# Optimization experiments

Hardware: AMD Instinct MI355X
Metric: run time of the kernel (lower is better)

The kernel has to match this reference:

```python
import jax, jax.numpy as jnp
import numpy as np

N = 200_000   # nodes
E = 6_400_000 # edges (avg degree 32)
G = 1024      # graphs in the batch
H = 8         # hidden dim


def setup_inputs() -> dict:
    key = jax.random.key(0)
    ks = jax.random.split(key, 13)
    x = jax.random.normal(ks[0], (N, 1), dtype=jnp.float32)
    edge_index = jax.random.randint(ks[1], (2, E), 0, N, dtype=jnp.int32)
    batch = jnp.sort(jax.random.randint(ks[2], (N,), 0, G, dtype=jnp.int32))
    s = 0.3
    params = dict(
        W1a=s * jax.random.normal(ks[3], (1, H), jnp.float32),
        b1a=jnp.zeros((H,), jnp.float32),
        W1b=s * jax.random.normal(ks[4], (H, H), jnp.float32),
        b1b=jnp.zeros((H,), jnp.float32),
        W2a=s * jax.random.normal(ks[5], (H, H), jnp.float32),
        b2a=jnp.zeros((H,), jnp.float32),
        W2b=s * jax.random.normal(ks[6], (H, H), jnp.float32),
        b2b=jnp.zeros((H,), jnp.float32),
        Wfc=s * jax.random.normal(ks[7], (H, 1), jnp.float32),
        bfc=jnp.zeros((1,), jnp.float32),
    )
    return dict(x=x, edge_index=edge_index, batch=batch, **params)


def _gin_layer(h, src, dst, Wa, ba, Wb, bb):
    # GINConv with eps=0: mlp(x_i + sum_{j->i} x_j); messages aggregated at dst=edge_index[1]
    agg = jax.ops.segment_sum(h[src], dst, num_segments=N)  # [N, d]
    z = h + agg
    z = jax.nn.relu(z @ Wa + ba)
    return z @ Wb + bb


def reference(x, edge_index, batch, W1a, b1a, W1b, b1b, W2a, b2a, W2b, b2b, Wfc, bfc):
    src, dst = edge_index[0], edge_index[1]
    h = _gin_layer(x, src, dst, W1a, b1a, W1b, b1b)   # [N, 8]
    h = jax.nn.elu(h)
    h = _gin_layer(h, src, dst, W2a, b2a, W2b, b2b)   # [N, 8]
    # global mean pool over graphs
    sums = jax.ops.segment_sum(h, batch, num_segments=G)                  # [G, 8]
    counts = jax.ops.segment_sum(jnp.ones((N,), h.dtype), batch, num_segments=G)
    pooled = sums / jnp.maximum(counts, 1.0)[:, None]
    out = jax.nn.sigmoid(pooled @ Wfc + bfc)          # [G, 1]
    return out.reshape(-1)
```

## Files before the change

kernel.cpp:

```cpp
#include <hip/hip_runtime.h>
#include <hip/hip_fp8.h>
#include <math.h>

#define H 8
#define NBLKA 256
#define BTH 1024
#define BSH 8
#define BCAP 9216
#define TS 1024
#define CAP 14336
#define SCAP 25600
#define POOLG 128

__device__ __forceinline__ unsigned f2fp8(float f) {
    __hip_fp8_e4m3 q(f);
    return (unsigned)q.__x;
}
__device__ __forceinline__ float fp8f(unsigned v) {
    __hip_fp8_e4m3 q;
    q.__x = (__hip_fp8_storage_t)v;
    return (float)q;
}
#if defined(__has_builtin)
#if __has_builtin(__builtin_amdgcn_cvt_pk_f32_fp8)
#define HAVE_CVT_PK_FP8 1
#endif
#endif
typedef float v2f __attribute__((ext_vector_type(2)));
__device__ __forceinline__ void unpack8(float* f, uint2 v) {
#ifdef HAVE_CVT_PK_FP8
    v2f f01 = __builtin_amdgcn_cvt_pk_f32_fp8((int)v.x, false);
    v2f f23 = __builtin_amdgcn_cvt_pk_f32_fp8((int)v.x, true);
    v2f f45 = __builtin_amdgcn_cvt_pk_f32_fp8((int)v.y, false);
    v2f f67 = __builtin_amdgcn_cvt_pk_f32_fp8((int)v.y, true);
    f[0] = f01.x; f[1] = f01.y; f[2] = f23.x; f[3] = f23.y;
    f[4] = f45.x; f[5] = f45.y; f[6] = f67.x; f[7] = f67.y;
#else
    f[0] = fp8f(v.x & 255u);         f[1] = fp8f((v.x >> 8) & 255u);
    f[2] = fp8f((v.x >> 16) & 255u); f[3] = fp8f(v.x >> 24);
    f[4] = fp8f(v.y & 255u);         f[5] = fp8f((v.y >> 8) & 255u);
    f[6] = fp8f((v.y >> 16) & 255u); f[7] = fp8f(v.y >> 24);
#endif
}
__device__ __forceinline__ void acc8(float* a, uint2 v) {
    float f[8];
    unpack8(f, v);
#pragma unroll
    for (int j = 0; j < 8; j++) a[j] += f[j];
}

__global__ __launch_bounds__(BTH) void scatterK(const int* __restrict__ ei, int E, int NB,
                                                int chunk, int* __restrict__ cursor,
                                                unsigned* __restrict__ packed) {
    __shared__ unsigned ss[SCAP];
    __shared__ int cnt[1024], sc[1024], base[1024], cur[1024];
    int t = threadIdx.x, blk = blockIdx.x;
    cnt[t] = 0;
    __syncthreads();
    int s = blk * chunk, e = min(E, s + chunk);
    for (int i = s + t; i < e; i += BTH)
        atomicAdd(&cnt[__builtin_nontemporal_load(ei + E + i) >> BSH], 1);
    __syncthreads();
    int c = cnt[t];
    sc[t] = c;
    __syncthreads();
    for (int off = 1; off < 1024; off <<= 1) {
        int v = (t >= off) ? sc[t - off] : 0;
        __syncthreads();
        sc[t] += v;
        __syncthreads();
    }
    cur[t] = sc[t] - c;
    base[t] = (t < NB && c > 0) ? atomicAdd(&cursor[t], c) : 0;
    __syncthreads();
    for (int i = s + t; i < e; i += BTH) {
        int src = __builtin_nontemporal_load(ei + i);
        int dst = __builtin_nontemporal_load(ei + E + i);
        int pos = atomicAdd(&cur[dst >> BSH], 1);
        ss[pos] = ((unsigned)src << 8) | (unsigned)(dst & 255);
    }
    __syncthreads();
    int wave = t >> 6, lane = t & 63;
    for (int j = wave; j < NB; j += (BTH >> 6)) {
        int n = cnt[j];
        int ls = sc[j] - n;
        int bs = base[j];
        int m = min(n, BCAP - bs);
        int gs = j * BCAP + bs;
        for (int k = lane; k < m; k += 64)
            packed[gs + k] = ss[ls + k];
    }
}

__global__ __launch_bounds__(TS, 8) void sortL1K(
                        unsigned* __restrict__ packed, const int* __restrict__ bucketCnt,
                        const float* __restrict__ x, int N,
                        const float* __restrict__ W1a, const float* __restrict__ b1a,
                        const float* __restrict__ W1b, const float* __restrict__ b1b,
                        int* __restrict__ nodeStart, uint2* __restrict__ h1) {
    __shared__ unsigned ss[CAP];
    __shared__ int cnt[256], sb[256], cur[256];
    __shared__ float sW1a[H], sb1a[H], sW1b[H * H], sb1b[H];
    int t = threadIdx.x, b = blockIdx.x;
    if (t < 256) cnt[t] = 0;
    else if (t < 256 + H) { int j = t - 256; sW1a[j] = W1a[j]; sb1a[j] = b1a[j]; sb1b[j] = b1b[j]; }
    else if (t < 256 + H + H * H) { int j = t - 256 - H; sW1b[j] = W1b[j]; }
    __syncthreads();
    int s = b * BCAP;
    int n_e = min(bucketCnt[b], BCAP);
    for (int i = t; i < n_e; i += TS)
        atomicAdd(&cnt[__builtin_nontemporal_load(packed + s + i) & 255u], 1);
    __syncthreads();
    if (t < 256) sb[t] = cnt[t];
    __syncthreads();
    for (int off = 1; off < 256; off <<= 1) {
        int add = (t < 256 && t >= off) ? sb[t - off] : 0;
        __syncthreads();
        if (t < 256) sb[t] += add;
        __syncthreads();
    }
    if (t < 256) {
        int excl = sb[t] - cnt[t];
        cur[t] = excl;
        nodeStart[(b << BSH) + t] = s + excl;
    }
    __syncthreads();
    for (int i = t; i < n_e; i += TS) {
        unsigned p = __builtin_nontemporal_load(packed + s + i);
        int pos = atomicAdd(&cur[p & 255u], 1);
        ss[pos] = p >> 8;
    }
    __syncthreads();
    for (int i = t; i < n_e; i += TS) packed[s + i] = ss[i];
    int node = t >> 2, q4 = t & 3;
    int gn = (b << BSH) + node;
    float xself = x[min(gn, N - 1)];
    int lo = sb[node] - cnt[node], hi = sb[node];
    float sum = 0.f;
    for (int k0 = lo + q4; k0 < hi; k0 += 32) {
        unsigned i0 = ss[k0];
        unsigned i1 = ss[min(k0 + 4,  hi - 1)];
        unsigned i2 = ss[min(k0 + 8,  hi - 1)];
        unsigned i3 = ss[min(k0 + 12, hi - 1)];
        unsigned i4 = ss[min(k0 + 16, hi - 1)];
        unsigned i5 = ss[min(k0 + 20, hi - 1)];
        unsigned i6 = ss[min(k0 + 24, hi - 1)];
        unsigned i7 = ss[min(k0 + 28, hi - 1)];
        float x0 = x[i0], x1 = x[i1], x2 = x[i2], x3 = x[i3];
        float x4 = x[i4], x5 = x[i5], x6 = x[i6], x7 = x[i7];
        sum += x0;
        if (k0 + 4  < hi) sum += x1;
        if (k0 + 8  < hi) sum += x2;
        if (k0 + 12 < hi) sum += x3;
        if (k0 + 16 < hi) sum += x4;
        if (k0 + 20 < hi) sum += x5;
        if (k0 + 24 < hi) sum += x6;
        if (k0 + 28 < hi) sum += x7;
    }
    sum += __shfl_xor(sum, 1, 64);
    sum += __shfl_xor(sum, 2, 64);
    if (q4 == 0 && gn < N) {
        float z = xself + sum;
        float tv[H];
#pragma unroll
        for (int k = 0; k < H; k++) tv[k] = fmaxf(fmaf(z, sW1a[k], sb1a[k]), 0.f);
        float hv[H];
#pragma unroll
        for (int j = 0; j < H; j++) {
            float a = sb1b[j];
#pragma unroll
            for (int k = 0; k < H; k++) a += tv[k] * sW1b[k * H + j];
            hv[j] = a > 0.f ? a : (expf(a) - 1.f);
        }
        uint2 o;
        o.x = f2fp8(hv[0]) | (f2fp8(hv[1]) << 8) | (f2fp8(hv[2]) << 16) | (f2fp8(hv[3]) << 24);
        o.y = f2fp8(hv[4]) | (f2fp8(hv[5]) << 8) | (f2fp8(hv[6]) << 16) | (f2fp8(hv[7]) << 24);
        h1[gn] = o;
    }
}

__global__ __launch_bounds__(1024, 8) void layer2K(
        const unsigned* __restrict__ packed, const int* __restrict__ nodeStart,
        const int* __restrict__ bucketCnt, const uint2* __restrict__ h1, int N,
        const float* __restrict__ W2a, const float* __restrict__ b2a,
        const float* __restrict__ W2b, const float* __restrict__ b2b,
        const int* __restrict__ batch, float* __restrict__ sumsCnt) {
    __shared__ unsigned ss[BCAP];
    __shared__ int sNS[257];
    __shared__ float pool[POOLG * 9];
    __shared__ float sW2a[H * H], sb2a[H], sW2b[H * H], sb2b[H];
    int t = threadIdx.x, b = blockIdx.x;
    int s = b * BCAP;
    int n_e = min(bucketCnt[b], BCAP);
    for (int i = t; i < n_e; i += 1024)
        ss[i] = __builtin_nontemporal_load(packed + s + i);
    if (t < 256) sNS[t] = nodeStart[(b << BSH) + t] - s;
    if (t == 256) sNS[256] = 0;
    if (t < H) { sb2a[t] = b2a[t]; sb2b[t] = b2b[t]; }
    else if (t >= 64 && t < 64 + H * H) sW2a[t - 64] = W2a[t - 64];
    else if (t >= 192 && t < 192 + H * H) sW2b[t - 192] = W2b[t - 192];
    __syncthreads();
    if (t == 0) sNS[256] = n_e;
    __syncthreads();
    int node = t >> 2, q4 = t & 3;
    int gn = (b << BSH) + node;
    uint2 vself = h1[gn];
    int lo = sNS[node], hi = sNS[node + 1];
    float a[H] = {0.f, 0.f, 0.f, 0.f, 0.f, 0.f, 0.f, 0.f};
    for (int k0 = lo + q4; k0 < hi; k0 += 32) {
        unsigned i0 = ss[k0];
        unsigned i1 = ss[min(k0 + 4,  hi - 1)];
        unsigned i2 = ss[min(k0 + 8,  hi - 1)];
        unsigned i3 = ss[min(k0 + 12, hi - 1)];
        unsigned i4 = ss[min(k0 + 16, hi - 1)];
        unsigned i5 = ss[min(k0 + 20, hi - 1)];
        unsigned i6 = ss[min(k0 + 24, hi - 1)];
        unsigned i7 = ss[min(k0 + 28, hi - 1)];
        uint2 v0 = h1[i0];
        uint2 v1 = h1[i1];
        uint2 v2 = h1[i2];
        uint2 v3 = h1[i3];
        uint2 v4 = h1[i4];
        uint2 v5 = h1[i5];
        uint2 v6 = h1[i6];
        uint2 v7 = h1[i7];
        acc8(a, v0);
        if (k0 + 4  < hi) acc8(a, v1);
        if (k0 + 8  < hi) acc8(a, v2);
        if (k0 + 12 < hi) acc8(a, v3);
        if (k0 + 16 < hi) acc8(a, v4);
        if (k0 + 20 < hi) acc8(a, v5);
        if (k0 + 24 < hi) acc8(a, v6);
        if (k0 + 28 < hi) acc8(a, v7);
    }
#pragma unroll
    for (int j = 0; j < H; j++) {
        a[j] += __shfl_xor(a[j], 1, 64);
        a[j] += __shfl_xor(a[j], 2, 64);
    }
    bool valid = (q4 == 0) && (gn < N);
    float h2[H];
    int g = 0;
    if (valid) {
        float zs[H];
        unpack8(zs, vself);
        float z[H];
#pragma unroll
        for (int j = 0; j < H; j++) z[j] = zs[j] + a[j];
        float tv[H];
#pragma unroll
        for (int k = 0; k < H; k++) {
            float acc = sb2a[k];
#pragma unroll
            for (int j = 0; j < H; j++) acc += z[j] * sW2a[j * H + k];
            tv[k] = fmaxf(acc, 0.f);
        }
#pragma unroll
        for (int j = 0; j < H; j++) {
            float acc = sb2b[j];
#pragma unroll
            for (int k = 0; k < H; k++) acc += tv[k] * sW2b[k * H + j];
            h2[j] = acc;
        }
        g = batch[gn];
    }
    int gfirst = batch[min(b << BSH, N - 1)];
    int glast  = batch[min((b << BSH) + 255, N - 1)];
    int span = glast - gfirst + 1;
    if (span <= POOLG) {
        int span9 = span * 9;
        for (int j = t; j < span9; j += 1024) pool[j] = 0.f;
        __syncthreads();
        if (valid) {
            float* p = &pool[(g - gfirst) * 9];
#pragma unroll
            for (int j = 0; j < H; j++) atomicAdd(p + j, h2[j]);
            atomicAdd(p + 8, 1.f);
        }
        __syncthreads();
        for (int j = t; j < span9; j += 1024)
            atomicAdd(&sumsCnt[(size_t)gfirst * 9 + j], pool[j]);
    } else if (valid) {
        float* p = &sumsCnt[(size_t)g * 9];
#pragma unroll
        for (int j = 0; j < H; j++) atomicAdd(p + j, h2[j]);
        atomicAdd(p + 8, 1.f);
    }
}

__global__ void finalK(const float* __restrict__ sumsCnt, const float* __restrict__ Wfc,
                       const float* __restrict__ bfc, float* __restrict__ out, int G) {
    int g = blockIdx.x * blockDim.x + threadIdx.x;
    if (g >= G) return;
    const float* s = &sumsCnt[(size_t)g * 9];
    float c = fmaxf(s[8], 1.f);
    float dot = 0.f;
#pragma unroll
    for (int j = 0; j < H; j++) dot += s[j] * Wfc[j];
    float a = dot / c + bfc[0];
    out[g] = 1.f / (1.f + expf(-a));
}

__global__ void edge_agg1(const int* __restrict__ ei, const float* __restrict__ x,
                          float* __restrict__ agg1, int E) {
    int e = blockIdx.x * blockDim.x + threadIdx.x;
    if (e >= E) return;
    atomicAdd(&agg1[ei[E + e]], x[ei[e]]);
}
__global__ void node1F(const float* __restrict__ x, const float* __restrict__ agg1,
                       const float* __restrict__ W1a, const float* __restrict__ b1a,
                       const float* __restrict__ W1b, const float* __restrict__ b1b,
                       float* __restrict__ h1, int N) {
    int n = blockIdx.x * blockDim.x + threadIdx.x;
    if (n >= N) return;
    float z = x[n] + agg1[n];
    float tv[H];
#pragma unroll
    for (int k = 0; k < H; k++) tv[k] = fmaxf(z * W1a[k] + b1a[k], 0.f);
#pragma unroll
    for (int j = 0; j < H; j++) {
        float acc = b1b[j];
#pragma unroll
        for (int k = 0; k < H; k++) acc += tv[k] * W1b[k * H + j];
        h1[(size_t)n * H + j] = acc > 0.f ? acc : (expf(acc) - 1.f);
    }
}
__global__ void edge_agg2(const int* __restrict__ ei, const float* __restrict__ h1,
                          float* __restrict__ agg2, int E) {
    long long i = (long long)blockIdx.x * blockDim.x + threadIdx.x;
    if (i >= (long long)E * H) return;
    int e = (int)(i >> 3), k = (int)(i & 7);
    atomicAdd(&agg2[(size_t)ei[E + e] * H + k], h1[(size_t)ei[e] * H + k]);
}
__global__ void node2F(const float* __restrict__ h1, const float* __restrict__ agg2,
                       const float* __restrict__ W2a, const float* __restrict__ b2a,
                       const float* __restrict__ W2b, const float* __restrict__ b2b,
                       const int* __restrict__ batch,
                       float* __restrict__ sums, float* __restrict__ counts, int N) {
    int n = blockIdx.x * blockDim.x + threadIdx.x;
    if (n >= N) return;
    float z[H], tv[H];
#pragma unroll
    for (int j = 0; j < H; j++) z[j] = h1[(size_t)n * H + j] + agg2[(size_t)n * H + j];
#pragma unroll
    for (int k = 0; k < H; k++) {
        float a = b2a[k];
#pragma unroll
        for (int j = 0; j < H; j++) a += z[j] * W2a[j * H + k];
        tv[k] = fmaxf(a, 0.f);
    }
    int g = batch[n];
#pragma unroll
    for (int j = 0; j < H; j++) {
        float a = b2b[j];
#pragma unroll
        for (int k = 0; k < H; k++) a += tv[k] * W2b[k * H + j];
        atomicAdd(&sums[(size_t)g * H + j], a);
    }
    atomicAdd(&counts[g], 1.f);
}
__global__ void finalF(const float* __restrict__ sums, const float* __restrict__ counts,
                       const float* __restrict__ Wfc, const float* __restrict__ bfc,
                       float* __restrict__ out, int G) {
    int g = blockIdx.x * blockDim.x + threadIdx.x;
    if (g >= G) return;
    float c = fmaxf(counts[g], 1.f);
    float acc = bfc[0];
#pragma unroll
    for (int j = 0; j < H; j++) acc += (sums[(size_t)g * H + j] / c) * Wfc[j];
    out[g] = 1.f / (1.f + expf(-acc));
}

extern "C" void kernel_launch(void* const* d_in, const int* in_sizes, int n_in,
                              void* d_out, int out_size, void* d_ws, size_t ws_size,
                              hipStream_t stream) {
    const float* x    = (const float*)d_in[0];
    const int*   ei   = (const int*)d_in[1];
    const int*   batch= (const int*)d_in[2];
    const float* W1a  = (const float*)d_in[3];
    const float* b1a  = (const float*)d_in[4];
    const float* W1b  = (const float*)d_in[5];
    const float* b1b  = (const float*)d_in[6];
    const float* W2a  = (const float*)d_in[7];
    const float* b2a  = (const float*)d_in[8];
    const float* W2b  = (const float*)d_in[9];
    const float* b2b  = (const float*)d_in[10];
    const float* Wfc  = (const float*)d_in[11];
    const float* bfc  = (const float*)d_in[12];

    const int N = in_sizes[0];
    const int E = in_sizes[1] / 2;
    const int G = out_size;
    const int NB = (N + 255) >> BSH;
    const int chunk = (E + NBLKA - 1) / NBLKA;
    const int B = 256;

    auto rnd4 = [](size_t v) { return (v + 3) & ~(size_t)3; };
    size_t o_cur  = 0;
    size_t o_sc   = 1024;
    size_t zelems = o_sc + (size_t)9 * G;
    size_t o_ns   = rnd4(zelems);
    size_t o_h1   = rnd4(o_ns + ((size_t)NB << BSH) + 1);
    size_t o_pk   = rnd4(o_h1 + ((size_t)NB << BSH) * 2);
    size_t total  = o_pk + (size_t)NB * BCAP;

    bool srcFits = (N <= (1 << 18));
    bool chunkFits = (chunk <= SCAP);
    bool capOK = ((size_t)E / NB) * 10 <= (size_t)BCAP * 9;
    if (NB <= 1024 && srcFits && chunkFits && capOK && ws_size >= total * 4) {
        int*      wsi = (int*)d_ws;
        float*    wsf = (float*)d_ws;
        unsigned* wsu = (unsigned*)d_ws;
        int*      cursor    = wsi + o_cur;
        float*    sumsCnt   = wsf + o_sc;
        int*      nodeStart = wsi + o_ns;
        uint2*    h1        = (uint2*)(wsu + o_h1);
        unsigned* packed    = wsu + o_pk;

        hipMemsetAsync(d_ws, 0, zelems * 4, stream);
        scatterK<<<NBLKA, BTH, 0, stream>>>(ei, E, NB, chunk, cursor, packed);
        sortL1K<<<NB, TS, 0, stream>>>(packed, cursor, x, N, W1a, b1a, W1b, b1b,
                                       nodeStart, h1);
        layer2K<<<NB, 1024, 0, stream>>>(packed, nodeStart, cursor, h1, N,
                                         W2a, b2a, W2b, b2b, batch, sumsCnt);
        finalK<<<(G + B - 1) / B, B, 0, stream>>>(sumsCnt, Wfc, bfc, (float*)d_out, G);
    } else {
        float* ws     = (float*)d_ws;
        float* agg1   = ws;
        float* agg2   = agg1 + (size_t)N;
        float* sums   = agg2 + (size_t)8 * N;
        float* counts = sums + (size_t)8 * G;
        float* h1     = counts + (size_t)G;
        hipMemsetAsync(ws, 0, ((size_t)9 * N + (size_t)9 * G) * sizeof(float), stream);
        edge_agg1<<<(E + B - 1) / B, B, 0, stream>>>(ei, x, agg1, E);
        node1F<<<(N + B - 1) / B, B, 0, stream>>>(x, agg1, W1a, b1a, W1b, b1b, h1, N);
        long long tot = (long long)E * H;
        edge_agg2<<<(int)((tot + B - 1) / B), B, 0, stream>>>(ei, h1, agg2, E);
        node2F<<<(N + B - 1) / B, B, 0, stream>>>(h1, agg2, W2a, b2a, W2b, b2b, batch,
                                                  sums, counts, N);
        finalF<<<(G + B - 1) / B, B, 0, stream>>>(sums, counts, Wfc, bfc, (float*)d_out, G);
    }
}
```

Before: 262.4 us.

## Fuse layer-1 aggregation into scatter and drop per-node sort via LDS atomics

Result: slower. 815.3 us (+210.7%).

```diff
diff --git a/kernel.cpp b/kernel.cpp
--- a/kernel.cpp
+++ b/kernel.cpp
@@ -7,8 +7,6 @@
 #define BTH 1024
 #define BSH 8
 #define BCAP 9216
-#define TS 1024
-#define CAP 14336
 #define SCAP 25600
 #define POOLG 128
 
@@ -42,16 +40,13 @@
     f[6] = fp8f((v.y >> 16) & 255u); f[7] = fp8f(v.y >> 24);
 #endif
 }
-__device__ __forceinline__ void acc8(float* a, uint2 v) {
-    float f[8];
-    unpack8(f, v);
-#pragma unroll
-    for (int j = 0; j < 8; j++) a[j] += f[j];
-}
-
-__global__ __launch_bounds__(BTH) void scatterK(const int* __restrict__ ei, int E, int NB,
-                                                int chunk, int* __restrict__ cursor,
-                                                unsigned* __restrict__ packed) {
+
+__global__ __launch_bounds__(BTH) void scatterK(const int* __restrict__ ei,
+                                                const float* __restrict__ x,
+                                                int E, int NB, int chunk,
+                                                int* __restrict__ cursor,
+                                                unsigned* __restrict__ packed,
+                                                float* __restrict__ agg1) {
     __shared__ unsigned ss[SCAP];
     __shared__ int cnt[1024], sc[1024], base[1024], cur[1024];
     int t = threadIdx.x, blk = blockIdx.x;
@@ -73,11 +68,31 @@
     cur[t] = sc[t] - c;
     base[t] = (t < NB && c > 0) ? atomicAdd(&cursor[t], c) : 0;
     __syncthreads();
-    for (int i = s + t; i < e; i += BTH) {
-        int src = __builtin_nontemporal_load(ei + i);
-        int dst = __builtin_nontemporal_load(ei + E + i);
-        int pos = atomicAdd(&cur[dst >> BSH], 1);
-        ss[pos] = ((unsigned)src << 8) | (unsigned)(dst & 255);
+    int i = s + t;
+    for (; i + 7 * BTH < e; i += 8 * BTH) {
+        int sv[8], dv[8];
+        float xv[8];
+#pragma unroll
+        for (int k = 0; k < 8; k++) {
+            sv[k] = __builtin_nontemporal_load(ei + i + k * BTH);
+            dv[k] = __builtin_nontemporal_load(ei + E + i + k * BTH);
+        }
+#pragma unroll
+        for (int k = 0; k < 8; k++) xv[k] = x[sv[k]];
+#pragma unroll
+        for (int k = 0; k < 8; k++) {
+            int pos = atomicAdd(&cur[dv[k] >> BSH], 1);
+            ss[pos] = ((unsigned)sv[k] << 8) | (unsigned)(dv[k] & 255);
+            atomicAdd(&agg1[dv[k]], xv[k]);
+        }
+    }
+    for (; i < e; i += BTH) {
+        int sv = __builtin_nontemporal_load(ei + i);
+        int dv = __builtin_nontemporal_load(ei + E + i);
+        float xv = x[sv];
+        int pos = atomicAdd(&cur[dv >> BSH], 1);
+        ss[pos] = ((unsigned)sv << 8) | (unsigned)(dv & 255);
+        atomicAdd(&agg1[dv], xv);
     }
     __syncthreads();
     int wave = t >> 6, lane = t & 63;
@@ -92,101 +107,49 @@
     }
 }
 
-__global__ __launch_bounds__(TS, 8) void sortL1K(
-                        unsigned* __restrict__ packed, const int* __restrict__ bucketCnt,
-                        const float* __restrict__ x, int N,
-                        const float* __restrict__ W1a, const float* __restrict__ b1a,
-                        const float* __restrict__ W1b, const float* __restrict__ b1b,
-                        int* __restrict__ nodeStart, uint2* __restrict__ h1) {
-    __shared__ unsigned ss[CAP];
-    __shared__ int cnt[256], sb[256], cur[256];
-    __shared__ float sW1a[H], sb1a[H], sW1b[H * H], sb1b[H];
-    int t = threadIdx.x, b = blockIdx.x;
-    if (t < 256) cnt[t] = 0;
-    else if (t < 256 + H) { int j = t - 256; sW1a[j] = W1a[j]; sb1a[j] = b1a[j]; sb1b[j] = b1b[j]; }
-    else if (t < 256 + H + H * H) { int j = t - 256 - H; sW1b[j] = W1b[j]; }
-    __syncthreads();
-    int s = b * BCAP;
-    int n_e = min(bucketCnt[b], BCAP);
-    for (int i = t; i < n_e; i += TS)
-        atomicAdd(&cnt[__builtin_nontemporal_load(packed + s + i) & 255u], 1);
-    __syncthreads();
-    if (t < 256) sb[t] = cnt[t];
-    __syncthreads();
-    for (int off = 1; off < 256; off <<= 1) {
-        int add = (t < 256 && t >= off) ? sb[t - off] : 0;
-        __syncthreads();
-        if (t < 256) sb[t] += add;
-        __syncthreads();
-    }
-    if (t < 256) {
-        int excl = sb[t] - cnt[t];
-        cur[t] = excl;
-        nodeStart[(b << BSH) + t] = s + excl;
-    }
-    __syncthreads();
-    for (int i = t; i < n_e; i += TS) {
-        unsigned p = __builtin_nontemporal_load(packed + s + i);
-        int pos = atomicAdd(&cur[p & 255u], 1);
-        ss[pos] = p >> 8;
-    }
-    __syncthreads();
-    for (int i = t; i < n_e; i += TS) packed[s + i] = ss[i];
-    int node = t >> 2, q4 = t & 3;
-    int gn = (b << BSH) + node;
-    float xself = x[min(gn, N - 1)];
-    int lo = sb[node] - cnt[node], hi = sb[node];
-    float sum = 0.f;
-    for (int k0 = lo + q4; k0 < hi; k0 += 32) {
-        unsigned i0 = ss[k0];
-        unsigned i1 = ss[min(k0 + 4,  hi - 1)];
-        unsigned i2 = ss[min(k0 + 8,  hi - 1)];
-        unsigned i3 = ss[min(k0 + 12, hi - 1)];
-        unsigned i4 = ss[min(k0 + 16, hi - 1)];
-        unsigned i5 = ss[min(k0 + 20, hi - 1)];
-        unsigned i6 = ss[min(k0 + 24, hi - 1)];
-        unsigned i7 = ss[min(k0 + 28, hi - 1)];
-        float x0 = x[i0], x1 = x[i1], x2 = x[i2], x3 = x[i3];
-        float x4 = x[i4], x5 = x[i5], x6 = x[i6], x7 = x[i7];
-        sum += x0;
-        if (k0 + 4  < hi) sum += x1;
-        if (k0 + 8  < hi) sum += x2;
-        if (k0 + 12 < hi) sum += x3;
-        if (k0 + 16 < hi) sum += x4;
-        if (k0 + 20 < hi) sum += x5;
-        if (k0 + 24 < hi) sum += x6;
-        if (k0 + 28 < hi) sum += x7;
-    }
-    sum += __shfl_xor(sum, 1, 64);
-    sum += __shfl_xor(sum, 2, 64);
-    if (q4 == 0 && gn < N) {
-        float z = xself + sum;
-        float tv[H];
-#pragma unroll
-        for (int k = 0; k < H; k++) tv[k] = fmaxf(fmaf(z, sW1a[k], sb1a[k]), 0.f);
-        float hv[H];
-#pragma unroll
-        for (int j = 0; j < H; j++) {
-            float a = sb1b[j];
-#pragma unroll
-            for (int k = 0; k < H; k++) a += tv[k] * sW1b[k * H + j];
-            hv[j] = a > 0.f ? a : (expf(a) - 1.f);
-        }
-        uint2 o;
-        o.x = f2fp8(hv[0]) | (f2fp8(hv[1]) << 8) | (f2fp8(hv[2]) << 16) | (f2fp8(hv[3]) << 24);
-        o.y = f2fp8(hv[4]) | (f2fp8(hv[5]) << 8) | (f2fp8(hv[6]) << 16) | (f2fp8(hv[7]) << 24);
-        h1[gn] = o;
-    }
+__global__ void node1K(const float* __restrict__ x, const float* __restrict__ agg1,
+                       const float* __restrict__ W1a, const float* __restrict__ b1a,
+                       const float* __restrict__ W1b, const float* __restrict__ b1b,
+                       uint2* __restrict__ h1, int N) {
+    int n = blockIdx.x * blockDim.x + threadIdx.x;
+    if (n >= N) return;
+    float z = x[n] + agg1[n];
+    float tv[H];
+#pragma unroll
+    for (int k = 0; k < H; k++) tv[k] = fmaxf(fmaf(z, W1a[k], b1a[k]), 0.f);
+    float hv[H];
+#pragma unroll
+    for (int j = 0; j < H; j++) {
+        float a = b1b[j];
+#pragma unroll
+        for (int k = 0; k < H; k++) a += tv[k] * W1b[k * H + j];
+        hv[j] = a > 0.f ? a : (expf(a) - 1.f);
+    }
+    uint2 o;
+    o.x = f2fp8(hv[0]) | (f2fp8(hv[1]) << 8) | (f2fp8(hv[2]) << 16) | (f2fp8(hv[3]) << 24);
+    o.y = f2fp8(hv[4]) | (f2fp8(hv[5]) << 8) | (f2fp8(hv[6]) << 16) | (f2fp8(hv[7]) << 24);
+    h1[n] = o;
+}
+
+__device__ __forceinline__ void edgeAdd(float* acc2, unsigned p, unsigned long long v) {
+    uint2 u;
+    u.x = (unsigned)v;
+    u.y = (unsigned)(v >> 32);
+    float f[8];
+    unpack8(f, u);
+    int d = (int)(p & 255u);
+#pragma unroll
+    for (int j = 0; j < 8; j++) atomicAdd(&acc2[j * 256 + d], f[j]);
 }
 
 __global__ __launch_bounds__(1024, 8) void layer2K(
-        const unsigned* __restrict__ packed, const int* __restrict__ nodeStart,
-        const int* __restrict__ bucketCnt, const uint2* __restrict__ h1, int N,
+        const unsigned* __restrict__ packed, const int* __restrict__ bucketCnt,
+        const uint2* __restrict__ h1, int N,
         const float* __restrict__ W2a, const float* __restrict__ b2a,
         const float* __restrict__ W2b, const float* __restrict__ b2b,
         const int* __restrict__ batch, float* __restrict__ sumsCnt) {
     __shared__ unsigned ss[BCAP];
-    __shared__ int sNS[257];
+    __shared__ float acc2[8 * 256];
     __shared__ float pool[POOLG * 9];
     __shared__ float sW2a[H * H], sb2a[H], sW2b[H * H], sb2b[H];
     int t = threadIdx.x, b = blockIdx.x;
@@ -194,59 +157,36 @@
     int n_e = min(bucketCnt[b], BCAP);
     for (int i = t; i < n_e; i += 1024)
         ss[i] = __builtin_nontemporal_load(packed + s + i);
-    if (t < 256) sNS[t] = nodeStart[(b << BSH) + t] - s;
-    if (t == 256) sNS[256] = 0;
+    for (int i = t; i < 8 * 256; i += 1024) acc2[i] = 0.f;
     if (t < H) { sb2a[t] = b2a[t]; sb2b[t] = b2b[t]; }
     else if (t >= 64 && t < 64 + H * H) sW2a[t - 64] = W2a[t - 64];
     else if (t >= 192 && t < 192 + H * H) sW2b[t - 192] = W2b[t - 192];
     __syncthreads();
-    if (t == 0) sNS[256] = n_e;
-    __syncthreads();
-    int node = t >> 2, q4 = t & 3;
-    int gn = (b << BSH) + node;
-    uint2 vself = h1[gn];
-    int lo = sNS[node], hi = sNS[node + 1];
-    float a[H] = {0.f, 0.f, 0.f, 0.f, 0.f, 0.f, 0.f, 0.f};
-    for (int k0 = lo + q4; k0 < hi; k0 += 32) {
-        unsigned i0 = ss[k0];
-        unsigned i1 = ss[min(k0 + 4,  hi - 1)];
-        unsigned i2 = ss[min(k0 + 8,  hi - 1)];
-        unsigned i3 = ss[min(k0 + 12, hi - 1)];
-        unsigned i4 = ss[min(k0 + 16, hi - 1)];
-        unsigned i5 = ss[min(k0 + 20, hi - 1)];
-        unsigned i6 = ss[min(k0 + 24, hi - 1)];
-        unsigned i7 = ss[min(k0 + 28, hi - 1)];
-        uint2 v0 = h1[i0];
-        uint2 v1 = h1[i1];
-        uint2 v2 = h1[i2];
-        uint2 v3 = h1[i3];
-        uint2 v4 = h1[i4];
-        uint2 v5 = h1[i5];
-        uint2 v6 = h1[i6];
-        uint2 v7 = h1[i7];
-        acc8(a, v0);
-        if (k0 + 4  < hi) acc8(a, v1);
-        if (k0 + 8  < hi) acc8(a, v2);
-        if (k0 + 12 < hi) acc8(a, v3);
-        if (k0 + 16 < hi) acc8(a, v4);
-        if (k0 + 20 < hi) acc8(a, v5);
-        if (k0 + 24 < hi) acc8(a, v6);
-        if (k0 + 28 < hi) acc8(a, v7);
-    }
-#pragma unroll
-    for (int j = 0; j < H; j++) {
-        a[j] += __shfl_xor(a[j], 1, 64);
-        a[j] += __shfl_xor(a[j], 2, 64);
-    }
-    bool valid = (q4 == 0) && (gn < N);
+    if (n_e > 0) {
+        unsigned pk[9];
+        unsigned long long vk[9];
+#pragma unroll
+        for (int k = 0; k < 9; k++)
+            pk[k] = ss[min(t + (k << 10), n_e - 1)];
+#pragma unroll
+        for (int k = 0; k < 9; k++)
+            vk[k] = *((const unsigned long long*)h1 + (pk[k] >> 8));
+#pragma unroll
+        for (int k = 0; k < 9; k++)
+            if (t + (k << 10) < n_e) edgeAdd(acc2, pk[k], vk[k]);
+    }
+    __syncthreads();
+    int gn = (b << BSH) + t;
+    bool valid = (t < 256) && (gn < N);
     float h2[H];
     int g = 0;
     if (valid) {
+        uint2 vs = h1[gn];
         float zs[H];
-        unpack8(zs, vself);
+        unpack8(zs, vs);
         float z[H];
 #pragma unroll
-        for (int j = 0; j < H; j++) z[j] = zs[j] + a[j];
+        for (int j = 0; j < H; j++) z[j] = zs[j] + acc2[j * 256 + t];
         float tv[H];
 #pragma unroll
         for (int k = 0; k < H; k++) {
@@ -398,9 +338,9 @@
     auto rnd4 = [](size_t v) { return (v + 3) & ~(size_t)3; };
     size_t o_cur  = 0;
     size_t o_sc   = 1024;
-    size_t zelems = o_sc + (size_t)9 * G;
-    size_t o_ns   = rnd4(zelems);
-    size_t o_h1   = rnd4(o_ns + ((size_t)NB << BSH) + 1);
+    size_t o_ag   = o_sc + (size_t)9 * G;
+    size_t zelems = o_ag + (size_t)N;
+    size_t o_h1   = rnd4(zelems);
     size_t o_pk   = rnd4(o_h1 + ((size_t)NB << BSH) * 2);
     size_t total  = o_pk + (size_t)NB * BCAP;
 
@@ -413,15 +353,14 @@
         unsigned* wsu = (unsigned*)d_ws;
         int*      cursor    = wsi + o_cur;
         float*    sumsCnt   = wsf + o_sc;
-        int*      nodeStart = wsi + o_ns;
+        float*    agg1      = wsf + o_ag;
         uint2*    h1        = (uint2*)(wsu + o_h1);
         unsigned* packed    = wsu + o_pk;
 
         hipMemsetAsync(d_ws, 0, zelems * 4, stream);
-        scatterK<<<NBLKA, BTH, 0, stream>>>(ei, E, NB, chunk, cursor, packed);
-        sortL1K<<<NB, TS, 0, stream>>>(packed, cursor, x, N, W1a, b1a, W1b, b1b,
-                                       nodeStart, h1);
-        layer2K<<<NB, 1024, 0, stream>>>(packed, nodeStart, cursor, h1, N,
+        scatterK<<<NBLKA, BTH, 0, stream>>>(ei, x, E, NB, chunk, cursor, packed, agg1);
+        node1K<<<(N + B - 1) / B, B, 0, stream>>>(x, agg1, W1a, b1a, W1b, b1b, h1, N);
+        layer2K<<<NB, 1024, 0, stream>>>(packed, cursor, h1, N,
                                          W2a, b2a, W2b, b2b, batch, sumsCnt);
         finalK<<<(G + B - 1) / B, B, 0, stream>>>(sumsCnt, Wfc, bfc, (float*)d_out, G);
     } else {
```
